# Kernel optimization log

Hardware: AMD Instinct MI355X
Metric: run time of the kernel (lower is better)

Reference implementation:

```python
import jax, jax.numpy as jnp
import numpy as np

TEMP1, TEMP2, TEMP3 = 4.0, 5.0, 10.0
NORM_EPS = 1e-12   # F.normalize eps
COS_EPS = 1e-8     # custom_cosine_similarity eps


def setup_inputs() -> dict:
    key = jax.random.key(0)
    k1, k2 = jax.random.split(key)
    vis_embeds = jax.random.normal(k1, (16, 16, 16, 16, 128), dtype=jnp.float32)
    txt_embeds = jax.random.normal(k2, (16, 64, 128), dtype=jnp.float32)
    return {"vis_embeds": vis_embeds, "txt_embeds": txt_embeds}


def reference(vis_embeds, txt_embeds):
    # vis_embeds: [bs, h, w, d, E]; txt_embeds: [bs, T, E] (uniform token_len)
    bs, h, w, d, E = vis_embeds.shape
    S = h * w * d
    # L2-normalize along embedding dim (F.normalize)
    vn = vis_embeds / jnp.clip(jnp.linalg.norm(vis_embeds, axis=-1, keepdims=True), NORM_EPS)
    vn = vn.reshape(bs, S, E)                      # context, flattened source
    tn = txt_embeds / jnp.clip(jnp.linalg.norm(txt_embeds, axis=-1, keepdims=True), NORM_EPS)
    # attention_fn, vectorized over the outer loop index i (txt sample):
    # attn0[i,b,s,t] = <context_b[s], query_i[t]>
    attn0 = jnp.einsum('bse,ite->ibst', vn, tn)    # [bs_txt, bs_vis, S, T]
    s1 = jax.nn.softmax(attn0, axis=-1)            # softmax over query tokens t
    a = jax.nn.softmax(TEMP1 * jnp.swapaxes(s1, -1, -2), axis=-1)  # [i,b,t,s], softmax over s
    # weighted context: [i,b,t,E]
    wc = jnp.einsum('ibts,bse->ibte', a, vn)
    # custom cosine similarity along E between txt tokens and weighted context
    num = jnp.einsum('ibte,ite->ibt', wc, tn)
    w1 = jnp.linalg.norm(tn, axis=-1)              # [i,t] (== 1 up to normalize eps)
    w2 = jnp.linalg.norm(wc, axis=-1)              # [i,b,t]
    cos = num / jnp.clip(w1[:, None, :] * w2, COS_EPS)
    # row_sim: mul temp2, exp, sum over tokens (agg='sum'), log
    row = jnp.log(jnp.sum(jnp.exp(TEMP2 * cos), axis=-1))  # [i_txt, b_vis]
    sims = row.T * TEMP3                           # [b_vis, i_txt] matches torch cat(dim=1)
    labels = jnp.arange(bs)
    logp0 = jax.nn.log_softmax(sims, axis=-1)
    logp1 = jax.nn.log_softmax(sims.T, axis=-1)
    loss0 = -jnp.mean(logp0[labels, labels])
    loss1 = -jnp.mean(logp1[labels, labels])
    loss = (loss0 + loss1) / 2.0
    # att_maps: for sample i the original keeps attn[i] -> diagonal of [i,b,...]
    att_maps = a[labels, labels].reshape(bs, -1, h, w, d)  # [bs, T, h, w, d]
    return loss, att_maps
```

## Files before the change

kernel.cpp:

```cpp
#include <hip/hip_runtime.h>

constexpr int BS = 16;
constexpr int S  = 4096;
constexpr int E  = 128;
constexpr int T  = 64;
constexpr int CH = 256;
constexpr int NCH = S / CH;
constexpr int VTS = 264;
constexpr int ETS = 264;
constexpr int TNS = 136;

typedef __attribute__((ext_vector_type(8))) short bf16x8;
typedef __attribute__((ext_vector_type(4))) float f32x4;

__device__ __forceinline__ unsigned short f2bf(float x) {
    unsigned u = __float_as_uint(x);
    u += 0x7FFFu + ((u >> 16) & 1u);
    return (unsigned short)(u >> 16);
}
__device__ __forceinline__ float bf2f(unsigned short v) {
    return __uint_as_float(((unsigned)v) << 16);
}

__global__ __launch_bounds__(1024, 4)
void clip_main_kernel(const float* __restrict__ vis,
                      const float* __restrict__ txt,
                      float* __restrict__ d_out,
                      float* __restrict__ ws)
{
    __shared__ unsigned short Vt[128 * VTS];
    __shared__ unsigned short ET[T * ETS];
    __shared__ unsigned short tnL[T * TNS];
    __shared__ float invn[CH];
    __shared__ float sinvt[T];
    __shared__ float scr[1024];

    const int tid = threadIdx.x;
    const int w   = tid >> 6;
    const int l   = tid & 63;
    const int cl  = l & 15;
    const int q   = l >> 4;
    const int b   = blockIdx.x & 15;
    const int i   = blockIdx.x >> 4;
    const bool diag = (i == b);

    {
        const int r   = tid >> 4;
        const int seg = tid & 15;
        const float* tp = txt + ((long)i * T + r) * E + (seg << 3);
        const float4 a0 = *(const float4*)(tp);
        const float4 a1 = *(const float4*)(tp + 4);
        float ssq = a0.x*a0.x + a0.y*a0.y + a0.z*a0.z + a0.w*a0.w
                  + a1.x*a1.x + a1.y*a1.y + a1.z*a1.z + a1.w*a1.w;
        ssq += __shfl_xor(ssq, 1); ssq += __shfl_xor(ssq, 2);
        ssq += __shfl_xor(ssq, 4); ssq += __shfl_xor(ssq, 8);
        const float inv = 1.0f / fmaxf(sqrtf(ssq), 1e-12f);
        if (seg == 0) sinvt[r] = inv;
        bf16x8 f;
        f[0]=(short)f2bf(a0.x*inv); f[1]=(short)f2bf(a0.y*inv);
        f[2]=(short)f2bf(a0.z*inv); f[3]=(short)f2bf(a0.w*inv);
        f[4]=(short)f2bf(a1.x*inv); f[5]=(short)f2bf(a1.y*inv);
        f[6]=(short)f2bf(a1.z*inv); f[7]=(short)f2bf(a1.w*inv);
        *(bf16x8*)&tnL[r * TNS + (seg << 3)] = f;
    }

    f32x4 acc2[2];
    acc2[0] = (f32x4){0.f,0.f,0.f,0.f};
    acc2[1] = (f32x4){0.f,0.f,0.f,0.f};
    const int et = w >> 1;
    const int nb = (w & 1) << 1;
    float dn[16];
#pragma unroll
    for (int k = 0; k < 16; ++k) dn[k] = 0.f;

    const float* visb = vis + (long)b * S * E;
    float* attb = d_out + 1 + (long)b * (long)T * S;

    for (int ch = 0; ch < NCH; ++ch) {
        const int s0 = ch * CH;

        {
            const int pp = tid >> 3, ee = tid & 7;
            const float* rA = visb + (long)(s0 + (pp << 1)) * E + (ee << 1);
            float2 va[8], vb[8];
            float sa = 0.f, sb = 0.f;
#pragma unroll
            for (int k = 0; k < 8; ++k) {
                va[k] = *(const float2*)(rA + (k << 4));
                vb[k] = *(const float2*)(rA + E + (k << 4));
                sa = fmaf(va[k].x, va[k].x, fmaf(va[k].y, va[k].y, sa));
                sb = fmaf(vb[k].x, vb[k].x, fmaf(vb[k].y, vb[k].y, sb));
            }
            sa += __shfl_xor(sa, 1); sa += __shfl_xor(sa, 2); sa += __shfl_xor(sa, 4);
            sb += __shfl_xor(sb, 1); sb += __shfl_xor(sb, 2); sb += __shfl_xor(sb, 4);
            const float ia = 1.0f / fmaxf(sqrtf(sa), 1e-12f);
            const float ib = 1.0f / fmaxf(sqrtf(sb), 1e-12f);
            if (ee == 0) { invn[pp << 1] = ia; invn[(pp << 1) + 1] = ib; }
#pragma unroll
            for (int k = 0; k < 8; ++k) {
                const int e0 = (ee << 1) + (k << 4);
                unsigned lo = (unsigned)f2bf(va[k].x * ia) | ((unsigned)f2bf(vb[k].x * ib) << 16);
                unsigned hi = (unsigned)f2bf(va[k].y * ia) | ((unsigned)f2bf(vb[k].y * ib) << 16);
                *(unsigned*)&Vt[e0 * VTS + (pp << 1)]       = lo;
                *(unsigned*)&Vt[(e0 + 1) * VTS + (pp << 1)] = hi;
            }
        }
        __syncthreads();

        f32x4 acc1[4];
#pragma unroll
        for (int mt = 0; mt < 4; ++mt) acc1[mt] = (f32x4){0.f,0.f,0.f,0.f};
        {
            const float* rowp = visb + (long)(s0 + (w << 4) + cl) * E + (q << 3);
            const float invr = invn[(w << 4) + cl];
#pragma unroll
            for (int kk = 0; kk < 4; ++kk) {
                const float4 a0 = *(const float4*)(rowp + (kk << 5));
                const float4 a1 = *(const float4*)(rowp + (kk << 5) + 4);
                bf16x8 Bf;
                Bf[0]=(short)f2bf(a0.x*invr); Bf[1]=(short)f2bf(a0.y*invr);
                Bf[2]=(short)f2bf(a0.z*invr); Bf[3]=(short)f2bf(a0.w*invr);
                Bf[4]=(short)f2bf(a1.x*invr); Bf[5]=(short)f2bf(a1.y*invr);
                Bf[6]=(short)f2bf(a1.z*invr); Bf[7]=(short)f2bf(a1.w*invr);
#pragma unroll
                for (int mt = 0; mt < 4; ++mt) {
                    const bf16x8 tAk = *(const bf16x8*)&tnL[((mt << 4) + cl) * TNS + (kk << 5) + (q << 3)];
                    acc1[mt] = __builtin_amdgcn_mfma_f32_16x16x32_bf16(tAk, Bf, acc1[mt], 0, 0, 0);
                }
            }
        }

        {
            float ex[4][4];
            float ssum = 0.f;
#pragma unroll
            for (int mt = 0; mt < 4; ++mt)
#pragma unroll
                for (int r = 0; r < 4; ++r) {
                    const float v = __expf(acc1[mt][r]);
                    ex[mt][r] = v; ssum += v;
                }
            ssum += __shfl_xor(ssum, 16);
            ssum += __shfl_xor(ssum, 32);
            const float csc = 4.0f / ssum;
            const int sloc = (w << 4) + cl;
#pragma unroll
            for (int mt = 0; mt < 4; ++mt)
#pragma unroll
                for (int r = 0; r < 4; ++r) {
                    const float e = __expf(ex[mt][r] * csc);
                    ET[((mt << 4) + (q << 2) + r) * ETS + sloc] = f2bf(e);
                    dn[(mt << 2) + r] += e;
                }
        }
        __syncthreads();

#pragma unroll
        for (int kk2 = 0; kk2 < 8; ++kk2) {
            const bf16x8 aV  = *(const bf16x8*)&Vt[((et << 4) + cl) * VTS + (kk2 << 5) + (q << 3)];
            const bf16x8 bE0 = *(const bf16x8*)&ET[((nb << 4) + cl) * ETS + (kk2 << 5) + (q << 3)];
            const bf16x8 bE1 = *(const bf16x8*)&ET[(((nb + 1) << 4) + cl) * ETS + (kk2 << 5) + (q << 3)];
            acc2[0] = __builtin_amdgcn_mfma_f32_16x16x32_bf16(aV, bE0, acc2[0], 0, 0, 0);
            acc2[1] = __builtin_amdgcn_mfma_f32_16x16x32_bf16(aV, bE1, acc2[1], 0, 0, 0);
        }

        if (diag) {
            const int tb = (tid >> 8) << 4;
            const int sl = tid & 255;
#pragma unroll
            for (int j = 0; j < 16; ++j)
                attb[(long)(tb + j) * S + s0 + sl] = bf2f(ET[(tb + j) * ETS + sl]);
        }
        __syncthreads();
    }

    if (diag) {
#pragma unroll
        for (int k = 0; k < 16; ++k) {
            dn[k] += __shfl_xor(dn[k], 1); dn[k] += __shfl_xor(dn[k], 2);
            dn[k] += __shfl_xor(dn[k], 4); dn[k] += __shfl_xor(dn[k], 8);
        }
        if (cl == 0) {
#pragma unroll
            for (int mt = 0; mt < 4; ++mt)
#pragma unroll
                for (int r = 0; r < 4; ++r)
                    scr[(w << 6) + (mt << 4) + (q << 2) + r] = dn[(mt << 2) + r];
        }
    }
    __syncthreads();
    if (diag && tid < 64) {
        float s = 0.f;
#pragma unroll
        for (int m = 0; m < 16; ++m) s += scr[(m << 6) + tid];
        ws[256 + (b << 6) + tid] = s;
    }
    __syncthreads();

    {
        float pn[2] = {0.f, 0.f}, pw[2] = {0.f, 0.f};
        int tloc[2];
#pragma unroll
        for (int j = 0; j < 2; ++j) {
            const int t = ((nb + j) << 4) + cl;
            tloc[j] = t;
            const float tinv = sinvt[t];
            const float* tp = txt + ((long)i * T + t) * E + (et << 4) + (q << 2);
#pragma unroll
            for (int r = 0; r < 4; ++r) {
                const float wc = acc2[j][r];
                const float tv = tp[r] * tinv;
                pn[j] = fmaf(wc, tv, pn[j]);
                pw[j] = fmaf(wc, wc, pw[j]);
            }
        }
#pragma unroll
        for (int j = 0; j < 2; ++j) {
            pn[j] += __shfl_xor(pn[j], 16); pn[j] += __shfl_xor(pn[j], 32);
            pw[j] += __shfl_xor(pw[j], 16); pw[j] += __shfl_xor(pw[j], 32);
        }
        if (q == 0) {
#pragma unroll
            for (int j = 0; j < 2; ++j) {
                scr[(et << 6) + tloc[j]]       = pn[j];
                scr[512 + (et << 6) + tloc[j]] = pw[j];
            }
        }
        __syncthreads();
        if (tid < 64) {
            float num = 0.f, w2 = 0.f;
#pragma unroll
            for (int m = 0; m < 8; ++m) {
                num += scr[(m << 6) + tid];
                w2  += scr[512 + (m << 6) + tid];
            }
            const float cosv = num / fmaxf(sqrtf(w2), 1e-20f);
            float r = __expf(5.0f * cosv);
#pragma unroll
            for (int m = 1; m < 64; m <<= 1) r += __shfl_xor(r, m);
            if (tid == 0) ws[(b << 4) + i] = 10.0f * logf(r);
        }
    }
}

__global__ __launch_bounds__(256, 4)
void att_norm_kernel(float* __restrict__ d_out, const float* __restrict__ ws)
{
    const int bt = blockIdx.x;
    const float inv = 1.0f / ws[256 + bt];
    float* pout = d_out + 1 + (long)bt * 4096;
#pragma unroll
    for (int k = 0; k < 16; ++k)
        pout[k * 256 + threadIdx.x] *= inv;
}

__global__ __launch_bounds__(256, 1)
void loss_kernel(const float* __restrict__ ws, float* __restrict__ d_out)
{
    __shared__ float sm[16][17];
    __shared__ float red[16];
    const int tid = threadIdx.x;
    const int bb = tid >> 4, ii = tid & 15;
    const float x = ws[bb * 16 + ii];
    sm[bb][ii] = x;

    float m = x;
#pragma unroll
    for (int msk = 1; msk < 16; msk <<= 1) m = fmaxf(m, __shfl_xor(m, msk));
    float s = __expf(x - m);
#pragma unroll
    for (int msk = 1; msk < 16; msk <<= 1) s += __shfl_xor(s, msk);
    const float lsm0 = x - m - logf(s);

    __syncthreads();
    const float y = sm[ii][bb];
    float m1 = y;
#pragma unroll
    for (int msk = 1; msk < 16; msk <<= 1) m1 = fmaxf(m1, __shfl_xor(m1, msk));
    float s1 = __expf(y - m1);
#pragma unroll
    for (int msk = 1; msk < 16; msk <<= 1) s1 += __shfl_xor(s1, msk);
    const float lsm1 = y - m1 - logf(s1);

    if (bb == ii) red[bb] = lsm0 + lsm1;
    __syncthreads();
    if (tid == 0) {
        float tot = 0.f;
#pragma unroll
        for (int k = 0; k < 16; ++k) tot += red[k];
        d_out[0] = -tot / 32.0f;
    }
}

extern "C" void kernel_launch(void* const* d_in, const int* in_sizes, int n_in,
                              void* d_out, int out_size, void* d_ws, size_t ws_size,
                              hipStream_t stream)
{
    const float* vis = (const float*)d_in[0];
    const float* txt = (const float*)d_in[1];
    float* out = (float*)d_out;
    float* ws  = (float*)d_ws;

    hipLaunchKernelGGL(clip_main_kernel, dim3(BS * BS), dim3(1024), 0, stream,
                       vis, txt, out, ws);
    hipLaunchKernelGGL(att_norm_kernel, dim3(BS * T), dim3(256), 0, stream, out, ws);
    hipLaunchKernelGGL(loss_kernel, dim3(1), dim3(256), 0, stream, ws, out);
}
```

Measured before the change: 228.2 us.

## Precompute normalized bf16 visual embeddings and transpose in a prep kernel

Adds a prep kernel that L2-normalizes the visual embeddings once per batch and writes both row-major and transposed bf16 copies to workspace. Previously each of the 256 blocks re-read the fp32 visual data and renormalized it. The main kernel now streams bf16 directly from global memory for both MFMA stages, doubles the chunk size to 512, and drops the shared-memory transpose buffer. The attention-map denominator is now computed in the normalization kernel from the stored values, not accumulated in the main kernel. The cost is an extra launch plus a workspace round trip, and the second-stage operand now comes from global or L2 memory rather than LDS.

New measurement: 243.0 us. 1.06x slower.

```diff
diff --git a/kernel.cpp b/kernel.cpp
--- a/kernel.cpp
+++ b/kernel.cpp
@@ -4,11 +4,15 @@
 constexpr int S  = 4096;
 constexpr int E  = 128;
 constexpr int T  = 64;
-constexpr int CH = 256;
+constexpr int CH = 512;
 constexpr int NCH = S / CH;
-constexpr int VTS = 264;
-constexpr int ETS = 264;
+constexpr int ETS = 520;
 constexpr int TNS = 136;
+constexpr int PTS = 264;
+
+constexpr long VN_OFF  = 0;
+constexpr long VNT_OFF = (long)BS * S * E;
+constexpr long WS_F    = (long)BS * S * E;
 
 typedef __attribute__((ext_vector_type(8))) short bf16x8;
 typedef __attribute__((ext_vector_type(4))) float f32x4;
@@ -23,17 +27,65 @@
 }
 
 __global__ __launch_bounds__(1024, 4)
-void clip_main_kernel(const float* __restrict__ vis,
+void prep_kernel(const float* __restrict__ vis, unsigned short* __restrict__ wsv)
+{
+    __shared__ unsigned short Lt[128 * PTS];
+    const int tid  = threadIdx.x;
+    const int b    = blockIdx.x >> 4;
+    const int tile = blockIdx.x & 15;
+    const int s0   = tile * 256;
+    const float* visb = vis + ((long)b * S + s0) * E;
+    unsigned short* vn  = wsv + VN_OFF  + ((long)b * S + s0) * E;
+    unsigned short* vnT = wsv + VNT_OFF + (long)b * E * S;
+
+    {
+        const int pp = tid >> 3, ee = tid & 7;
+        const float* rA = visb + (long)(pp << 1) * E + (ee << 1);
+        float2 va[8], vb[8];
+        float sa = 0.f, sb = 0.f;
+#pragma unroll
+        for (int k = 0; k < 8; ++k) {
+            va[k] = *(const float2*)(rA + (k << 4));
+            vb[k] = *(const float2*)(rA + E + (k << 4));
+            sa = fmaf(va[k].x, va[k].x, fmaf(va[k].y, va[k].y, sa));
+            sb = fmaf(vb[k].x, vb[k].x, fmaf(vb[k].y, vb[k].y, sb));
+        }
+        sa += __shfl_xor(sa, 1); sa += __shfl_xor(sa, 2); sa += __shfl_xor(sa, 4);
+        sb += __shfl_xor(sb, 1); sb += __shfl_xor(sb, 2); sb += __shfl_xor(sb, 4);
+        const float ia = 1.0f / fmaxf(sqrtf(sa), 1e-12f);
+        const float ib = 1.0f / fmaxf(sqrtf(sb), 1e-12f);
+        const long r0 = (long)(pp << 1) * E, r1 = r0 + E;
+#pragma unroll
+        for (int k = 0; k < 8; ++k) {
+            const int e0 = (ee << 1) + (k << 4);
+            const unsigned ax = f2bf(va[k].x * ia), ay = f2bf(va[k].y * ia);
+            const unsigned bx = f2bf(vb[k].x * ib), by = f2bf(vb[k].y * ib);
+            *(unsigned*)&Lt[e0 * PTS + (pp << 1)]       = ax | (bx << 16);
+            *(unsigned*)&Lt[(e0 + 1) * PTS + (pp << 1)] = ay | (by << 16);
+            *(unsigned*)&vn[r0 + e0] = ax | (ay << 16);
+            *(unsigned*)&vn[r1 + e0] = bx | (by << 16);
+        }
+    }
+    __syncthreads();
+    {
+        const int e = tid >> 3, sseg = (tid & 7) << 5;
+#pragma unroll
+        for (int k = 0; k < 4; ++k) {
+            const bf16x8 v = *(const bf16x8*)&Lt[e * PTS + sseg + (k << 3)];
+            *(bf16x8*)&vnT[(long)e * S + s0 + sseg + (k << 3)] = v;
+        }
+    }
+}
+
+__global__ __launch_bounds__(1024, 4)
+void clip_main_kernel(const unsigned short* __restrict__ wsv,
                       const float* __restrict__ txt,
                       float* __restrict__ d_out,
-                      float* __restrict__ ws)
-{
-    __shared__ unsigned short Vt[128 * VTS];
+                      float* __restrict__ wsf)
+{
     __shared__ unsigned short ET[T * ETS];
     __shared__ unsigned short tnL[T * TNS];
-    __shared__ float invn[CH];
-    __shared__ float sinvt[T];
-    __shared__ float scr[1024];
+    __shared__ float scrA[512], scrB[512];
 
     const int tid = threadIdx.x;
     const int w   = tid >> 6;
@@ -45,8 +97,7 @@
     const bool diag = (i == b);
 
     {
-        const int r   = tid >> 4;
-        const int seg = tid & 15;
+        const int r = tid >> 4, seg = tid & 15;
         const float* tp = txt + ((long)i * T + r) * E + (seg << 3);
         const float4 a0 = *(const float4*)(tp);
         const float4 a1 = *(const float4*)(tp + 4);
@@ -55,7 +106,6 @@
         ssq += __shfl_xor(ssq, 1); ssq += __shfl_xor(ssq, 2);
         ssq += __shfl_xor(ssq, 4); ssq += __shfl_xor(ssq, 8);
         const float inv = 1.0f / fmaxf(sqrtf(ssq), 1e-12f);
-        if (seg == 0) sinvt[r] = inv;
         bf16x8 f;
         f[0]=(short)f2bf(a0.x*inv); f[1]=(short)f2bf(a0.y*inv);
         f[2]=(short)f2bf(a0.z*inv); f[3]=(short)f2bf(a0.w*inv);
@@ -63,167 +113,112 @@
         f[6]=(short)f2bf(a1.z*inv); f[7]=(short)f2bf(a1.w*inv);
         *(bf16x8*)&tnL[r * TNS + (seg << 3)] = f;
     }
+    __syncthreads();
 
     f32x4 acc2[2];
     acc2[0] = (f32x4){0.f,0.f,0.f,0.f};
     acc2[1] = (f32x4){0.f,0.f,0.f,0.f};
-    const int et = w >> 1;
-    const int nb = (w & 1) << 1;
-    float dn[16];
-#pragma unroll
-    for (int k = 0; k < 16; ++k) dn[k] = 0.f;
-
-    const float* visb = vis + (long)b * S * E;
+    const int et  = w >> 1;
+    const int ntb = (w & 1) << 1;
+
+    const unsigned short* vnb  = wsv + VN_OFF  + (long)b * S * E;
+    const unsigned short* vntb = wsv + VNT_OFF + (long)b * E * S;
     float* attb = d_out + 1 + (long)b * (long)T * S;
 
     for (int ch = 0; ch < NCH; ++ch) {
         const int s0 = ch * CH;
 
+        f32x4 acc1[2][4];
+#pragma unroll
+        for (int st = 0; st < 2; ++st)
+#pragma unroll
+            for (int mt = 0; mt < 4; ++mt) acc1[st][mt] = (f32x4){0.f,0.f,0.f,0.f};
         {
-            const int pp = tid >> 3, ee = tid & 7;
-            const float* rA = visb + (long)(s0 + (pp << 1)) * E + (ee << 1);
-            float2 va[8], vb[8];
-            float sa = 0.f, sb = 0.f;
-#pragma unroll
-            for (int k = 0; k < 8; ++k) {
-                va[k] = *(const float2*)(rA + (k << 4));
-                vb[k] = *(const float2*)(rA + E + (k << 4));
-                sa = fmaf(va[k].x, va[k].x, fmaf(va[k].y, va[k].y, sa));
-                sb = fmaf(vb[k].x, vb[k].x, fmaf(vb[k].y, vb[k].y, sb));
-            }
-            sa += __shfl_xor(sa, 1); sa += __shfl_xor(sa, 2); sa += __shfl_xor(sa, 4);
-            sb += __shfl_xor(sb, 1); sb += __shfl_xor(sb, 2); sb += __shfl_xor(sb, 4);
-            const float ia = 1.0f / fmaxf(sqrtf(sa), 1e-12f);
-            const float ib = 1.0f / fmaxf(sqrtf(sb), 1e-12f);
-            if (ee == 0) { invn[pp << 1] = ia; invn[(pp << 1) + 1] = ib; }
-#pragma unroll
-            for (int k = 0; k < 8; ++k) {
-                const int e0 = (ee << 1) + (k << 4);
-                unsigned lo = (unsigned)f2bf(va[k].x * ia) | ((unsigned)f2bf(vb[k].x * ib) << 16);
-                unsigned hi = (unsigned)f2bf(va[k].y * ia) | ((unsigned)f2bf(vb[k].y * ib) << 16);
-                *(unsigned*)&Vt[e0 * VTS + (pp << 1)]       = lo;
-                *(unsigned*)&Vt[(e0 + 1) * VTS + (pp << 1)] = hi;
-            }
-        }
-        __syncthreads();
-
-        f32x4 acc1[4];
-#pragma unroll
-        for (int mt = 0; mt < 4; ++mt) acc1[mt] = (f32x4){0.f,0.f,0.f,0.f};
-        {
-            const float* rowp = visb + (long)(s0 + (w << 4) + cl) * E + (q << 3);
-            const float invr = invn[(w << 4) + cl];
+            const unsigned short* r0 = vnb + (long)(s0 + (w << 5) + cl) * E + (q << 3);
 #pragma unroll
             for (int kk = 0; kk < 4; ++kk) {
-                const float4 a0 = *(const float4*)(rowp + (kk << 5));
-                const float4 a1 = *(const float4*)(rowp + (kk << 5) + 4);
-                bf16x8 Bf;
-                Bf[0]=(short)f2bf(a0.x*invr); Bf[1]=(short)f2bf(a0.y*invr);
-                Bf[2]=(short)f2bf(a0.z*invr); Bf[3]=(short)f2bf(a0.w*invr);
-                Bf[4]=(short)f2bf(a1.x*invr); Bf[5]=(short)f2bf(a1.y*invr);
-                Bf[6]=(short)f2bf(a1.z*invr); Bf[7]=(short)f2bf(a1.w*invr);
+                const bf16x8 Bf0 = *(const bf16x8*)(r0 + (kk << 5));
+                const bf16x8 Bf1 = *(const bf16x8*)(r0 + 16 * E + (kk << 5));
 #pragma unroll
                 for (int mt = 0; mt < 4; ++mt) {
                     const bf16x8 tAk = *(const bf16x8*)&tnL[((mt << 4) + cl) * TNS + (kk << 5) + (q << 3)];
-                    acc1[mt] = __builtin_amdgcn_mfma_f32_16x16x32_bf16(tAk, Bf, acc1[mt], 0, 0, 0);
+                    acc1[0][mt] = __builtin_amdgcn_mfma_f32_16x16x32_bf16(tAk, Bf0, acc1[0][mt], 0, 0, 0);
+                    acc1[1][mt] = __builtin_amdgcn_mfma_f32_16x16x32_bf16(tAk, Bf1, acc1[1][mt], 0, 0, 0);
                 }
             }
         }
 
-        {
+#pragma unroll
+        for (int st = 0; st < 2; ++st) {
             float ex[4][4];
             float ssum = 0.f;
 #pragma unroll
             for (int mt = 0; mt < 4; ++mt)
 #pragma unroll
                 for (int r = 0; r < 4; ++r) {
-                    const float v = __expf(acc1[mt][r]);
+                    const float v = __expf(acc1[st][mt][r]);
                     ex[mt][r] = v; ssum += v;
                 }
             ssum += __shfl_xor(ssum, 16);
             ssum += __shfl_xor(ssum, 32);
             const float csc = 4.0f / ssum;
-            const int sloc = (w << 4) + cl;
+            const int sloc = (w << 5) + (st << 4) + cl;
 #pragma unroll
             for (int mt = 0; mt < 4; ++mt)
 #pragma unroll
-                for (int r = 0; r < 4; ++r) {
-                    const float e = __expf(ex[mt][r] * csc);
-                    ET[((mt << 4) + (q << 2) + r) * ETS + sloc] = f2bf(e);
-                    dn[(mt << 2) + r] += e;
-                }
+                for (int r = 0; r < 4; ++r)
+                    ET[((mt << 4) + (q << 2) + r) * ETS + sloc] = f2bf(__expf(ex[mt][r] * csc));
         }
         __syncthreads();
 
-#pragma unroll
-        for (int kk2 = 0; kk2 < 8; ++kk2) {
-            const bf16x8 aV  = *(const bf16x8*)&Vt[((et << 4) + cl) * VTS + (kk2 << 5) + (q << 3)];
-            const bf16x8 bE0 = *(const bf16x8*)&ET[((nb << 4) + cl) * ETS + (kk2 << 5) + (q << 3)];
-            const bf16x8 bE1 = *(const bf16x8*)&ET[(((nb + 1) << 4) + cl) * ETS + (kk2 << 5) + (q << 3)];
-            acc2[0] = __builtin_amdgcn_mfma_f32_16x16x32_bf16(aV, bE0, acc2[0], 0, 0, 0);
-            acc2[1] = __builtin_amdgcn_mfma_f32_16x16x32_bf16(aV, bE1, acc2[1], 0, 0, 0);
+        {
+            const unsigned short* ar = vntb + (long)((et << 4) + cl) * S + s0 + (q << 3);
+            const unsigned short* b0 = &ET[((ntb << 4) + cl) * ETS + (q << 3)];
+            const unsigned short* b1 = &ET[(((ntb + 1) << 4) + cl) * ETS + (q << 3)];
+#pragma unroll
+            for (int kk2 = 0; kk2 < 16; ++kk2) {
+                const bf16x8 aV  = *(const bf16x8*)(ar + (kk2 << 5));
+                const bf16x8 bE0 = *(const bf16x8*)(b0 + (kk2 << 5));
+                const bf16x8 bE1 = *(const bf16x8*)(b1 + (kk2 << 5));
+                acc2[0] = __builtin_amdgcn_mfma_f32_16x16x32_bf16(aV, bE0, acc2[0], 0, 0, 0);
+                acc2[1] = __builtin_amdgcn_mfma_f32_16x16x32_bf16(aV, bE1, acc2[1], 0, 0, 0);
+            }
         }
 
         if (diag) {
-            const int tb = (tid >> 8) << 4;
-            const int sl = tid & 255;
-#pragma unroll
-            for (int j = 0; j < 16; ++j)
-                attb[(long)(tb + j) * S + s0 + sl] = bf2f(ET[(tb + j) * ETS + sl]);
+            const int t = tid >> 4, sb = (tid & 15) << 5;
+            float* ap = attb + (long)t * S + s0 + sb;
+#pragma unroll
+            for (int k = 0; k < 8; ++k) {
+                const ushort4 v = *(const ushort4*)&ET[t * ETS + sb + (k << 2)];
+                ap[(k << 2) + 0] = bf2f(v.x);
+                ap[(k << 2) + 1] = bf2f(v.y);
+                ap[(k << 2) + 2] = bf2f(v.z);
+                ap[(k << 2) + 3] = bf2f(v.w);
+            }
         }
         __syncthreads();
     }
-
-    if (diag) {
-#pragma unroll
-        for (int k = 0; k < 16; ++k) {
-            dn[k] += __shfl_xor(dn[k], 1); dn[k] += __shfl_xor(dn[k], 2);
-            dn[k] += __shfl_xor(dn[k], 4); dn[k] += __shfl_xor(dn[k], 8);
-        }
-        if (cl == 0) {
-#pragma unroll
-            for (int mt = 0; mt < 4; ++mt)
-#pragma unroll
-                for (int r = 0; r < 4; ++r)
-                    scr[(w << 6) + (mt << 4) + (q << 2) + r] = dn[(mt << 2) + r];
-        }
-    }
-    __syncthreads();
-    if (diag && tid < 64) {
-        float s = 0.f;
-#pragma unroll
-        for (int m = 0; m < 16; ++m) s += scr[(m << 6) + tid];
-        ws[256 + (b << 6) + tid] = s;
-    }
-    __syncthreads();
 
     {
         float pn[2] = {0.f, 0.f}, pw[2] = {0.f, 0.f};
-        int tloc[2];
 #pragma unroll
         for (int j = 0; j < 2; ++j) {
-            const int t = ((nb + j) << 4) + cl;
-            tloc[j] = t;
-            const float tinv = sinvt[t];
-            const float* tp = txt + ((long)i * T + t) * E + (et << 4) + (q << 2);
-#pragma unroll
-            for (int r = 0; r < 4; ++r) {
-                const float wc = acc2[j][r];
-                const float tv = tp[r] * tinv;
-                pn[j] = fmaf(wc, tv, pn[j]);
-                pw[j] = fmaf(wc, wc, pw[j]);
-            }
-        }
-#pragma unroll
-        for (int j = 0; j < 2; ++j) {
+            const int t = ((ntb + j) << 4) + cl;
+            const ushort4 tns = *(const ushort4*)&tnL[t * TNS + (et << 4) + (q << 2)];
+            const float tv0 = bf2f(tns.x), tv1 = bf2f(tns.y), tv2 = bf2f(tns.z), tv3 = bf2f(tns.w);
+            pn[j] = acc2[j][0]*tv0 + acc2[j][1]*tv1 + acc2[j][2]*tv2 + acc2[j][3]*tv3;
+            pw[j] = acc2[j][0]*acc2[j][0] + acc2[j][1]*acc2[j][1]
+                  + acc2[j][2]*acc2[j][2] + acc2[j][3]*acc2[j][3];
             pn[j] += __shfl_xor(pn[j], 16); pn[j] += __shfl_xor(pn[j], 32);
             pw[j] += __shfl_xor(pw[j], 16); pw[j] += __shfl_xor(pw[j], 32);
         }
         if (q == 0) {
 #pragma unroll
             for (int j = 0; j < 2; ++j) {
-                scr[(et << 6) + tloc[j]]       = pn[j];
-                scr[512 + (et << 6) + tloc[j]] = pw[j];
+                const int t = ((ntb + j) << 4) + cl;
+                scrA[(et << 6) + t] = pn[j];
+                scrB[(et << 6) + t] = pw[j];
             }
         }
         __syncthreads();
@@ -231,37 +226,46 @@
             float num = 0.f, w2 = 0.f;
 #pragma unroll
             for (int m = 0; m < 8; ++m) {
-                num += scr[(m << 6) + tid];
-                w2  += scr[512 + (m << 6) + tid];
+                num += scrA[(m << 6) + tid];
+                w2  += scrB[(m << 6) + tid];
             }
             const float cosv = num / fmaxf(sqrtf(w2), 1e-20f);
             float r = __expf(5.0f * cosv);
 #pragma unroll
             for (int m = 1; m < 64; m <<= 1) r += __shfl_xor(r, m);
-            if (tid == 0) ws[(b << 4) + i] = 10.0f * logf(r);
+            if (tid == 0) wsf[WS_F + (b << 4) + i] = 10.0f * logf(r);
         }
     }
 }
 
 __global__ __launch_bounds__(256, 4)
-void att_norm_kernel(float* __restrict__ d_out, const float* __restrict__ ws)
-{
+void att_norm_kernel(float* __restrict__ d_out)
+{
+    __shared__ float r4[4];
+    const int tid = threadIdx.x;
     const int bt = blockIdx.x;
-    const float inv = 1.0f / ws[256 + bt];
-    float* pout = d_out + 1 + (long)bt * 4096;
-#pragma unroll
-    for (int k = 0; k < 16; ++k)
-        pout[k * 256 + threadIdx.x] *= inv;
+    float* p = d_out + 1 + (long)bt * 4096;
+    float v[16];
+    float s = 0.f;
+#pragma unroll
+    for (int k = 0; k < 16; ++k) { v[k] = p[k * 256 + tid]; s += v[k]; }
+#pragma unroll
+    for (int m = 1; m < 64; m <<= 1) s += __shfl_xor(s, m);
+    if ((tid & 63) == 0) r4[tid >> 6] = s;
+    __syncthreads();
+    const float inv = 1.0f / (r4[0] + r4[1] + r4[2] + r4[3]);
+#pragma unroll
+    for (int k = 0; k < 16; ++k) p[k * 256 + tid] = v[k] * inv;
 }
 
 __global__ __launch_bounds__(256, 1)
-void loss_kernel(const float* __restrict__ ws, float* __restrict__ d_out)
+void loss_kernel(const float* __restrict__ wsf, float* __restrict__ d_out)
 {
     __shared__ float sm[16][17];
     __shared__ float red[16];
     const int tid = threadIdx.x;
     const int bb = tid >> 4, ii = tid & 15;
-    const float x = ws[bb * 16 + ii];
+    const float x = wsf[WS_F + bb * 16 + ii];
     sm[bb][ii] = x;
 
     float m = x;
@@ -299,10 +303,12 @@
     const float* vis = (const float*)d_in[0];
     const float* txt = (const float*)d_in[1];
     float* out = (float*)d_out;
-    float* ws  = (float*)d_ws;
-
+    unsigned short* wsv = (unsigned short*)d_ws;
+    float* wsf = (float*)d_ws;
+
+    hipLaunchKernelGGL(prep_kernel, dim3(256), dim3(1024), 0, stream, vis, wsv);
     hipLaunchKernelGGL(clip_main_kernel, dim3(BS * BS), dim3(1024), 0, stream,
-                       vis, txt, out, ws);
-    hipLaunchKernelGGL(att_norm_kernel, dim3(BS * T), dim3(256), 0, stream, out, ws);
-    hipLaunchKernelGGL(loss_kernel, dim3(1), dim3(256), 0, stream, ws, out);
-}
+                       wsv, txt, out, wsf);
+    hipLaunchKernelGGL(att_norm_kernel, dim3(BS * T), dim3(256), 0, stream, out);
+    hipLaunchKernelGGL(loss_kernel, dim3(1), dim3(256), 0, stream, wsf, out);
+}
```
